# Kernel optimization log

Measured on AMD Instinct MI355X. Metric: run time of the kernel, lower is better.

## Reference

```python
import jax, jax.numpy as jnp
import numpy as np

B, C, E, TOPK = 8192, 1024, 8, 4
H = 4 * C  # mlp_ratio = 4.0
EPS = 1e-6


def quick_gelu(x):
    return x * jax.nn.sigmoid(1.702 * x)


def layer_norm(x, gamma, beta):
    mu = jnp.mean(x, axis=-1, keepdims=True)
    var = jnp.var(x, axis=-1, keepdims=True)
    return (x - mu) * jax.lax.rsqrt(var + EPS) * gamma + beta


def setup_inputs() -> dict:
    key = jax.random.key(0)
    ks = jax.random.split(key, 8)
    s1 = 1.0 / np.sqrt(C)
    s2 = 1.0 / np.sqrt(H)
    return {
        "x": jax.random.normal(ks[0], (B, C), dtype=jnp.float32),
        "W1": jax.random.uniform(ks[1], (E, C, H), jnp.float32, -s1, s1),
        "b1": jax.random.uniform(ks[2], (E, H), jnp.float32, -s1, s1),
        "W2": jax.random.uniform(ks[3], (E, H, C), jnp.float32, -s2, s2),
        "b2": jax.random.uniform(ks[4], (E, C), jnp.float32, -s2, s2),
        "ln_g": jnp.ones((E, C), jnp.float32),
        "ln_b": jnp.zeros((E, C), jnp.float32),
        "Wg": jax.random.uniform(ks[5], (C, E), jnp.float32, -s1, s1),
        "bg": jax.random.uniform(ks[6], (E,), jnp.float32, -s1, s1),
    }


def reference(x, W1, b1, W2, b2, ln_g, ln_b, Wg, bg):
    # gate + softmax + top-k
    scores = jax.nn.softmax(x @ Wg + bg, axis=-1)           # [B, E]
    topk_scores, topk_idx = jax.lax.top_k(scores, TOPK)     # [B, K]
    # all experts on all tokens (naive MoE, matches original)
    h = quick_gelu(jnp.einsum('bc,ech->beh', x, W1) + b1)   # [B, E, H]
    y = quick_gelu(jnp.einsum('beh,ehc->bec', h, W2) + b2)  # [B, E, C]
    y = layer_norm(y, ln_g, ln_b)                            # [B, E, C]
    # gather top-k expert outputs and weighted-combine
    topk_out = jnp.take_along_axis(y, topk_idx[:, :, None], axis=1)  # [B, K, C]
    return jnp.sum(topk_out * topk_scores[:, :, None], axis=1)       # [B, C]
```

## Files before the change

### kernel.cpp

```cpp
#include <hip/hip_runtime.h>

#define NB 8192
#define NC 1024
#define NE 8
#define NK 4
#define NH 4096
constexpr int ROWCAP = NB * NK + NE * 128;

typedef _Float16 f16;
typedef _Float16 f16x8 __attribute__((ext_vector_type(8)));
typedef _Float16 f16x4 __attribute__((ext_vector_type(4)));
typedef float    f32x4 __attribute__((ext_vector_type(4)));

__device__ __forceinline__ void async_cp16(const f16* g, f16* l) {
    __builtin_amdgcn_global_load_lds((const __attribute__((address_space(1))) void*)g,
                                     (__attribute__((address_space(3))) void*)l, 16, 0, 0);
}

__device__ __forceinline__ float quick_gelu(float v) {
    return v / (1.f + __expf(-1.702f * v));
}

__global__ void cast_x_k(const float* __restrict__ x, f16* __restrict__ x16) {
    int i = blockIdx.x * 256 + threadIdx.x;
    float4 v = ((const float4*)x)[i];
    f16x4 h = { (f16)v.x, (f16)v.y, (f16)v.z, (f16)v.w };
    ((f16x4*)x16)[i] = h;
}

__global__ void transpose_cast_k(const float* __restrict__ in, f16* __restrict__ out,
                                 int R, int S) {
    __shared__ f16 tile[32][33];
    int e = blockIdx.z;
    long base = (long)e * R * S;
    int s0 = blockIdx.x * 32, r0 = blockIdx.y * 32;
    int tx = threadIdx.x & 31, ty = threadIdx.x >> 5;
    #pragma unroll
    for (int i = 0; i < 32; i += 8)
        tile[ty + i][tx] = (f16)in[base + (long)(r0 + ty + i) * S + s0 + tx];
    __syncthreads();
    #pragma unroll
    for (int i = 0; i < 32; i += 8)
        out[base + (long)(s0 + ty + i) * R + r0 + tx] = tile[tx][ty + i];
}

__global__ void gating_k(const float* __restrict__ x, const float* __restrict__ Wg,
                         const float* __restrict__ bg, int* __restrict__ counts,
                         int* __restrict__ tokmap, int* __restrict__ eids,
                         int* __restrict__ slots, float* __restrict__ gatew) {
    int b = blockIdx.x, t = threadIdx.x;
    float acc[NE] = {};
    float4 xv = ((const float4*)(x + (long)b * NC))[t];
    const float* wr = Wg + (long)t * 4 * NE;
    #pragma unroll
    for (int j = 0; j < 4; j++) {
        float xj = ((const float*)&xv)[j];
        #pragma unroll
        for (int e2 = 0; e2 < NE; e2++) acc[e2] += xj * wr[j * NE + e2];
    }
    #pragma unroll
    for (int e2 = 0; e2 < NE; e2++)
        #pragma unroll
        for (int off = 32; off; off >>= 1) acc[e2] += __shfl_down(acc[e2], off);
    __shared__ float red[4][NE];
    int lane = t & 63, w = t >> 6;
    if (lane == 0)
        for (int e2 = 0; e2 < NE; e2++) red[w][e2] = acc[e2];
    __syncthreads();
    if (t == 0) {
        float l[NE];
        float m = -1e30f;
        for (int e2 = 0; e2 < NE; e2++) {
            l[e2] = red[0][e2] + red[1][e2] + red[2][e2] + red[3][e2] + bg[e2];
            m = fmaxf(m, l[e2]);
        }
        float p[NE], sum = 0.f;
        for (int e2 = 0; e2 < NE; e2++) { p[e2] = __expf(l[e2] - m); sum += p[e2]; }
        float inv = 1.f / sum;
        for (int e2 = 0; e2 < NE; e2++) p[e2] *= inv;
        bool taken[NE] = {};
        for (int k = 0; k < NK; k++) {
            int be = 0; float bv = -1e30f;
            for (int e2 = 0; e2 < NE; e2++)
                if (!taken[e2] && p[e2] > bv) { bv = p[e2]; be = e2; }
            taken[be] = true;
            int slot = atomicAdd(&counts[be], 1);
            tokmap[be * NB + slot] = b;
            eids[b * NK + k] = be;
            slots[b * NK + k] = slot;
            gatew[b * NK + k] = bv;
        }
    }
}

__global__ void offsets_k(const int* __restrict__ counts, int* __restrict__ offp) {
    if (threadIdx.x == 0 && blockIdx.x == 0) {
        int o = 0;
        for (int e = 0; e < NE; e++) { offp[e] = o; o += ((counts[e] + 127) >> 7) << 7; }
    }
}

__global__ __launch_bounds__(256) void gemm_f16(
    const f16* __restrict__ A, const f16* __restrict__ Bt,
    const float* __restrict__ bias, f16* __restrict__ Out,
    const int* __restrict__ counts, const int* __restrict__ offp,
    const int* __restrict__ tokmap, int Kd, int N, int gather) {
    int e = blockIdx.z;
    int cnt = counts[e];
    int m0 = blockIdx.x << 7;
    if (m0 >= cnt) return;
    int n0 = blockIdx.y << 7;
    int base = offp[e];

    __shared__ __align__(16) f16 At[128 * 32];
    __shared__ __align__(16) f16 Bs[128 * 32];

    int t = threadIdx.x;
    int lane = t & 63;
    int w = t >> 6;
    int wm = (w >> 1) << 6, wn = (w & 1) << 6;

    int sr = m0 + (t >> 2);
    int sc = (t & 3) << 3;
    int ca = sr < cnt - 1 ? sr : cnt - 1;
    int cb = sr + 64 < cnt - 1 ? sr + 64 : cnt - 1;
    long arow0, arow1;
    if (gather) { arow0 = tokmap[e * NB + ca]; arow1 = tokmap[e * NB + cb]; }
    else        { arow0 = base + ca;           arow1 = base + cb; }
    const f16* ap0 = A + arow0 * (long)Kd + sc;
    const f16* ap1 = A + arow1 * (long)Kd + sc;
    const f16* bp0 = Bt + ((long)e * N + n0 + (t >> 2)) * (long)Kd + sc;
    const f16* bp1 = bp0 + (long)64 * Kd;

    f32x4 acc[4][4] = {};
    int ml = lane & 15, kq = (lane >> 4) << 3;

    for (int k0 = 0; k0 < Kd; k0 += 32) {
        async_cp16(ap0 + k0, &At[t * 8]);
        async_cp16(ap1 + k0, &At[2048 + t * 8]);
        async_cp16(bp0 + k0, &Bs[t * 8]);
        async_cp16(bp1 + k0, &Bs[2048 + t * 8]);
        __syncthreads();
        f16x8 af[4], bf[4];
        #pragma unroll
        for (int mi = 0; mi < 4; mi++) af[mi] = *(const f16x8*)&At[(wm + mi * 16 + ml) * 32 + kq];
        #pragma unroll
        for (int ni = 0; ni < 4; ni++) bf[ni] = *(const f16x8*)&Bs[(wn + ni * 16 + ml) * 32 + kq];
        #pragma unroll
        for (int mi = 0; mi < 4; mi++)
            #pragma unroll
            for (int ni = 0; ni < 4; ni++)
                acc[mi][ni] = __builtin_amdgcn_mfma_f32_16x16x32_f16(af[mi], bf[ni], acc[mi][ni], 0, 0, 0);
        __syncthreads();
    }

    int rq = (lane >> 4) << 2;
    #pragma unroll
    for (int ni = 0; ni < 4; ni++) {
        int col = n0 + wn + ni * 16 + ml;
        float bv = bias[(long)e * N + col];
        #pragma unroll
        for (int mi = 0; mi < 4; mi++) {
            int r0 = m0 + wm + mi * 16 + rq;
            #pragma unroll
            for (int rr = 0; rr < 4; rr++) {
                int row = r0 + rr;
                if (row < cnt) {
                    float v = acc[mi][ni][rr] + bv;
                    Out[(long)(base + row) * N + col] = (f16)quick_gelu(v);
                }
            }
        }
    }
}

__global__ void ln_combine_k(const f16* __restrict__ y16, const float* __restrict__ lng,
                             const float* __restrict__ lnb, const int* __restrict__ eids,
                             const int* __restrict__ slots, const float* __restrict__ gatew,
                             const int* __restrict__ offp, float* __restrict__ out) {
    int b = blockIdx.x, t = threadIdx.x;
    int lane = t & 63, w = t >> 6;
    __shared__ float red[4][2];
    float o[4] = {0.f, 0.f, 0.f, 0.f};
    int c0 = t * 4;
    for (int k = 0; k < NK; k++) {
        int e = eids[b * NK + k];
        long r = offp[e] + slots[b * NK + k];
        float wk = gatew[b * NK + k];
        f16x4 hv = *(const f16x4*)(y16 + r * NC + c0);
        float v[4];
        #pragma unroll
        for (int j = 0; j < 4; j++) v[j] = (float)hv[j];
        float s = v[0] + v[1] + v[2] + v[3];
        float ss = v[0] * v[0] + v[1] * v[1] + v[2] * v[2] + v[3] * v[3];
        #pragma unroll
        for (int off = 32; off; off >>= 1) { s += __shfl_down(s, off); ss += __shfl_down(ss, off); }
        if (lane == 0) { red[w][0] = s; red[w][1] = ss; }
        __syncthreads();
        float S  = red[0][0] + red[1][0] + red[2][0] + red[3][0];
        float SS = red[0][1] + red[1][1] + red[2][1] + red[3][1];
        float mu = S * (1.f / NC);
        float var = SS * (1.f / NC) - mu * mu;
        float rs = rsqrtf(var + 1e-6f);
        #pragma unroll
        for (int j = 0; j < 4; j++) {
            float g  = lng[(long)e * NC + c0 + j];
            float bb = lnb[(long)e * NC + c0 + j];
            o[j] += wk * ((v[j] - mu) * rs * g + bb);
        }
        __syncthreads();
    }
    float4 ov = {o[0], o[1], o[2], o[3]};
    ((float4*)(out + (long)b * NC))[t] = ov;
}

extern "C" void kernel_launch(void* const* d_in, const int* in_sizes, int n_in,
                              void* d_out, int out_size, void* d_ws, size_t ws_size,
                              hipStream_t stream) {
    const float* x   = (const float*)d_in[0];
    const float* W1  = (const float*)d_in[1];
    const float* b1  = (const float*)d_in[2];
    const float* W2  = (const float*)d_in[3];
    const float* b2  = (const float*)d_in[4];
    const float* lng = (const float*)d_in[5];
    const float* lnb = (const float*)d_in[6];
    const float* Wg  = (const float*)d_in[7];
    const float* bg  = (const float*)d_in[8];
    float* out = (float*)d_out;

    char* ws = (char*)d_ws;
    size_t o = 0;
    auto take = [&](size_t bytes) { char* p = ws + o; o += (bytes + 255) & ~(size_t)255; return p; };
    f16*   x16    = (f16*)take((size_t)NB * NC * 2);
    f16*   w1t    = (f16*)take((size_t)NE * NH * NC * 2);
    f16*   w2t    = (f16*)take((size_t)NE * NC * NH * 2);
    f16*   h16    = (f16*)take((size_t)ROWCAP * NH * 2);
    f16*   y16    = (f16*)take((size_t)ROWCAP * NC * 2);
    int*   tokmap = (int*)take((size_t)NE * NB * 4);
    int*   eids   = (int*)take((size_t)NB * NK * 4);
    int*   slots  = (int*)take((size_t)NB * NK * 4);
    float* gatew  = (float*)take((size_t)NB * NK * 4);
    int*   counts = (int*)take(256);
    int*   offp   = (int*)take(256);

    hipMemsetAsync(counts, 0, NE * sizeof(int), stream);
    cast_x_k<<<NB * NC / 1024, 256, 0, stream>>>(x, x16);
    transpose_cast_k<<<dim3(NH / 32, NC / 32, NE), 256, 0, stream>>>(W1, w1t, NC, NH);
    transpose_cast_k<<<dim3(NC / 32, NH / 32, NE), 256, 0, stream>>>(W2, w2t, NH, NC);
    gating_k<<<NB, 256, 0, stream>>>(x, Wg, bg, counts, tokmap, eids, slots, gatew);
    offsets_k<<<1, 64, 0, stream>>>(counts, offp);
    gemm_f16<<<dim3(64, NH / 128, NE), 256, 0, stream>>>(x16, w1t, b1, h16, counts, offp, tokmap, NC, NH, 1);
    gemm_f16<<<dim3(64, NC / 128, NE), 256, 0, stream>>>(h16, w2t, b2, y16, counts, offp, tokmap, NH, NC, 0);
    ln_combine_k<<<NB, 256, 0, stream>>>(y16, lng, lnb, eids, slots, gatew, offp, out);
}
```

Before: 1.986 ms.

## Swizzle GEMM LDS layout, fuse x cast into gating, hoist LDS pointers

Applies an XOR swizzle to the 16-byte chunk column in the GEMM's LDS tiles, on both the async global-to-LDS store side and the fragment read side. This is meant to cut LDS bank conflicts when the MFMA operand fragments are read. The fp32-to-fp16 cast of x moves into the gating kernel, which already loads x, so one launch and one full pass over x go away. LDS and global pointers are also precomputed outside the k-loop to reduce address arithmetic. The swizzle must match exactly between the write and read sides, or the results will be wrong.

```diff
diff --git a/kernel.cpp b/kernel.cpp
--- a/kernel.cpp
+++ b/kernel.cpp
@@ -19,13 +19,6 @@
 
 __device__ __forceinline__ float quick_gelu(float v) {
     return v / (1.f + __expf(-1.702f * v));
-}
-
-__global__ void cast_x_k(const float* __restrict__ x, f16* __restrict__ x16) {
-    int i = blockIdx.x * 256 + threadIdx.x;
-    float4 v = ((const float4*)x)[i];
-    f16x4 h = { (f16)v.x, (f16)v.y, (f16)v.z, (f16)v.w };
-    ((f16x4*)x16)[i] = h;
 }
 
 __global__ void transpose_cast_k(const float* __restrict__ in, f16* __restrict__ out,
@@ -47,10 +40,13 @@
 __global__ void gating_k(const float* __restrict__ x, const float* __restrict__ Wg,
                          const float* __restrict__ bg, int* __restrict__ counts,
                          int* __restrict__ tokmap, int* __restrict__ eids,
-                         int* __restrict__ slots, float* __restrict__ gatew) {
+                         int* __restrict__ slots, float* __restrict__ gatew,
+                         f16* __restrict__ x16) {
     int b = blockIdx.x, t = threadIdx.x;
     float acc[NE] = {};
     float4 xv = ((const float4*)(x + (long)b * NC))[t];
+    f16x4 hx = { (f16)xv.x, (f16)xv.y, (f16)xv.z, (f16)xv.w };
+    ((f16x4*)(x16 + (long)b * NC))[t] = hx;
     const float* wr = Wg + (long)t * 4 * NE;
     #pragma unroll
     for (int j = 0; j < 4; j++) {
@@ -121,7 +117,7 @@
     int wm = (w >> 1) << 6, wn = (w & 1) << 6;
 
     int sr = m0 + (t >> 2);
-    int sc = (t & 3) << 3;
+    int sc = (((t & 3) ^ ((t >> 3) & 3)) << 3);
     int ca = sr < cnt - 1 ? sr : cnt - 1;
     int cb = sr + 64 < cnt - 1 ? sr + 64 : cnt - 1;
     long arow0, arow1;
@@ -133,19 +129,30 @@
     const f16* bp1 = bp0 + (long)64 * Kd;
 
     f32x4 acc[4][4] = {};
-    int ml = lane & 15, kq = (lane >> 4) << 3;
+    int ml = lane & 15;
+    int sxq = (((lane >> 4) ^ ((ml >> 1) & 3)) << 3);
+    const f16* ard[4];
+    const f16* brd[4];
+    #pragma unroll
+    for (int mi = 0; mi < 4; mi++) ard[mi] = &At[(wm + mi * 16 + ml) * 32 + sxq];
+    #pragma unroll
+    for (int ni = 0; ni < 4; ni++) brd[ni] = &Bs[(wn + ni * 16 + ml) * 32 + sxq];
+    f16* la0 = &At[t * 8];
+    f16* la1 = &At[2048 + t * 8];
+    f16* lb0 = &Bs[t * 8];
+    f16* lb1 = &Bs[2048 + t * 8];
 
     for (int k0 = 0; k0 < Kd; k0 += 32) {
-        async_cp16(ap0 + k0, &At[t * 8]);
-        async_cp16(ap1 + k0, &At[2048 + t * 8]);
-        async_cp16(bp0 + k0, &Bs[t * 8]);
-        async_cp16(bp1 + k0, &Bs[2048 + t * 8]);
+        async_cp16(ap0, la0); ap0 += 32;
+        async_cp16(ap1, la1); ap1 += 32;
+        async_cp16(bp0, lb0); bp0 += 32;
+        async_cp16(bp1, lb1); bp1 += 32;
         __syncthreads();
         f16x8 af[4], bf[4];
         #pragma unroll
-        for (int mi = 0; mi < 4; mi++) af[mi] = *(const f16x8*)&At[(wm + mi * 16 + ml) * 32 + kq];
-        #pragma unroll
-        for (int ni = 0; ni < 4; ni++) bf[ni] = *(const f16x8*)&Bs[(wn + ni * 16 + ml) * 32 + kq];
+        for (int mi = 0; mi < 4; mi++) af[mi] = *(const f16x8*)ard[mi];
+        #pragma unroll
+        for (int ni = 0; ni < 4; ni++) bf[ni] = *(const f16x8*)brd[ni];
         #pragma unroll
         for (int mi = 0; mi < 4; mi++)
             #pragma unroll
@@ -244,10 +251,9 @@
     int*   offp   = (int*)take(256);
 
     hipMemsetAsync(counts, 0, NE * sizeof(int), stream);
-    cast_x_k<<<NB * NC / 1024, 256, 0, stream>>>(x, x16);
     transpose_cast_k<<<dim3(NH / 32, NC / 32, NE), 256, 0, stream>>>(W1, w1t, NC, NH);
     transpose_cast_k<<<dim3(NC / 32, NH / 32, NE), 256, 0, stream>>>(W2, w2t, NH, NC);
-    gating_k<<<NB, 256, 0, stream>>>(x, Wg, bg, counts, tokmap, eids, slots, gatew);
+    gating_k<<<NB, 256, 0, stream>>>(x, Wg, bg, counts, tokmap, eids, slots, gatew, x16);
     offsets_k<<<1, 64, 0, stream>>>(counts, offp);
     gemm_f16<<<dim3(64, NH / 128, NE), 256, 0, stream>>>(x16, w1t, b1, h16, counts, offp, tokmap, NC, NH, 1);
     gemm_f16<<<dim3(64, NC / 128, NE), 256, 0, stream>>>(h16, w2t, b2, y16, counts, offp, tokmap, NH, NC, 0);
```

After: 1.921 ms. -3.2%, faster.
